# Optimization experiments

Measured on AMD Instinct MI355X. Metric: run time of the kernel, lower is better.

## Reference

```python
import jax, jax.numpy as jnp
import numpy as np

N_NODES = 50000
N_EDGES = 625000
D = 128


def setup_inputs() -> dict:
    key = jax.random.key(0)
    kx, ks, kr, kw, kb = jax.random.split(key, 5)
    x = jax.random.normal(kx, (N_NODES, D), dtype=jnp.float32)
    senders = jax.random.randint(ks, (N_EDGES,), 0, N_NODES, dtype=jnp.int64)
    receivers = jax.random.randint(kr, (N_EDGES,), 0, N_NODES, dtype=jnp.int64)
    # nn.Linear(2*D, D): weight [D, 2*D], bias [D]
    lim = 1.0 / np.sqrt(2 * D)
    W = jax.random.uniform(kw, (D, 2 * D), minval=-lim, maxval=lim, dtype=jnp.float32)
    b = jax.random.uniform(kb, (D,), minval=-lim, maxval=lim, dtype=jnp.float32)
    return {"x": x, "senders": senders, "receivers": receivers, "n_nodes": N_NODES, "W": W, "b": b}


def reference(x, senders, receivers, n_nodes, W, b):
    # Add self loops (with_self=True)
    self_idx = jnp.arange(n_nodes, dtype=senders.dtype)
    s = jnp.concatenate([senders, self_idx])   # [E + N]
    r = jnp.concatenate([receivers, self_idx]) # [E + N]

    ones = jnp.ones(r.shape[0], dtype=x.dtype)
    # degree_norm=True branch (note: mirrors the original's naming exactly:
    # 'out_degree' counted over receivers, 'in_degree' over senders)
    out_degree = jax.ops.segment_sum(ones, r, num_segments=n_nodes)  # [N]
    in_degree = jax.ops.segment_sum(ones, s, num_segments=n_nodes)   # [N]
    out_degree_norm = jax.lax.rsqrt(jnp.maximum(out_degree, 1.0))
    in_degree_norm = jax.lax.rsqrt(jnp.maximum(in_degree, 1.0))

    # Gather sender embeddings, scale, scatter-add to receivers
    sender_emb = x[s] * out_degree_norm[s][:, None]  # [E+N, D]
    aggregated = jax.ops.segment_sum(sender_emb, r, num_segments=n_nodes)  # [N, D]

    # edge_count over receivers == out_degree (same scatter), clamped
    edge_count = jnp.maximum(out_degree, 1.0)
    aggregated = aggregated / edge_count[:, None]
    aggregated = aggregated * in_degree_norm[:, None]

    combined = jnp.concatenate([x, aggregated], axis=1)  # [N, 2D]
    return combined @ W.T + b
```

## Files before the change

### kernel.cpp

```cpp
#include <hip/hip_runtime.h>

#define DIM 128
#define BM 128
#define BK 32
#define PAD 16

typedef __attribute__((ext_vector_type(8))) short short8;
typedef __attribute__((ext_vector_type(4))) float f32x4;

__device__ __forceinline__ unsigned short f2bf(float f) {
    unsigned int b = __float_as_uint(f);
    return (unsigned short)((b + 0x7fffu + ((b >> 16) & 1u)) >> 16);
}
__device__ __forceinline__ float bf_lo(unsigned int u) {
    return __uint_as_float(u << 16);
}
__device__ __forceinline__ float bf_hi(unsigned int u) {
    return __uint_as_float(u & 0xffff0000u);
}
__device__ __forceinline__ uint2 pack4(float4 v) {
    uint2 r;
    r.x = (unsigned int)f2bf(v.x) | ((unsigned int)f2bf(v.y) << 16);
    r.y = (unsigned int)f2bf(v.z) | ((unsigned int)f2bf(v.w) << 16);
    return r;
}

__global__ void prep_kernel(const float4* __restrict__ x4,
                            const float4* __restrict__ W4,
                            const int* __restrict__ senders,
                            const int* __restrict__ receivers,
                            uint2* __restrict__ xb4,
                            uint2* __restrict__ Wb4,
                            int* __restrict__ cnt_r_pad,
                            int* __restrict__ cnt_s_pad,
                            int* __restrict__ rank,
                            int nx4, int nw4, int E) {
    int i = blockIdx.x * blockDim.x + threadIdx.x;
    if (i < nw4) Wb4[i] = pack4(W4[i]);
    if (i < E) {
        int r = receivers[i];
        int s = senders[i];
        rank[i] = atomicAdd(&cnt_r_pad[r * PAD], 1);
        atomicAdd(&cnt_s_pad[s * PAD], 1);
    }
    if (i < nx4) xb4[i] = pack4(x4[i]);
}

__global__ __launch_bounds__(256) void scan_phase_a(const int* __restrict__ cnt_r_pad,
                                                    int* __restrict__ bsum, int N) {
    __shared__ int red[256];
    int t = threadIdx.x;
    int i = blockIdx.x * 256 + t;
    red[t] = (i < N) ? cnt_r_pad[i * PAD] : 0;
    __syncthreads();
    for (int s = 128; s > 0; s >>= 1) {
        if (t < s) red[t] += red[t + s];
        __syncthreads();
    }
    if (t == 0) bsum[blockIdx.x] = red[0];
}

__global__ __launch_bounds__(256) void scan_phase_b(const int* __restrict__ bsum,
                                                    int* __restrict__ boff, int NB) {
    __shared__ int sh[256];
    int t = threadIdx.x;
    int v = (t < NB) ? bsum[t] : 0;
    sh[t] = v;
    __syncthreads();
    for (int off = 1; off < 256; off <<= 1) {
        int u = (t >= off) ? sh[t - off] : 0;
        __syncthreads();
        sh[t] += u;
        __syncthreads();
    }
    if (t < NB) boff[t] = sh[t] - v;
}

__global__ __launch_bounds__(256) void scan_phase_c(const int* __restrict__ cnt_r_pad,
                                                    const int* __restrict__ cnt_s_pad,
                                                    const int* __restrict__ boff,
                                                    int* __restrict__ row_start,
                                                    float* __restrict__ sscale,
                                                    float2* __restrict__ fin2,
                                                    int N) {
    __shared__ int sh[256];
    int t = threadIdx.x;
    int i = blockIdx.x * 256 + t;
    int v = (i < N) ? cnt_r_pad[i * PAD] : 0;
    sh[t] = v;
    __syncthreads();
    for (int off = 1; off < 256; off <<= 1) {
        int u = (t >= off) ? sh[t - off] : 0;
        __syncthreads();
        sh[t] += u;
        __syncthreads();
    }
    if (i < N) {
        int excl = sh[t] - v + boff[blockIdx.x];
        row_start[i] = excl;
        if (i == N - 1) row_start[N] = excl + v;
        float od = (float)(v + 1);
        float onorm = rsqrtf(od);
        sscale[i] = onorm;
        int ds = cnt_s_pad[i * PAD];
        fin2[i] = make_float2(onorm, rsqrtf((float)(ds + 1)) / od);
    }
}

__global__ void fill_kernel(const int* __restrict__ senders,
                            const int* __restrict__ receivers,
                            const int* __restrict__ row_start,
                            const int* __restrict__ rank,
                            int* __restrict__ edge_src,
                            int E) {
    int e = blockIdx.x * blockDim.x + threadIdx.x;
    if (e < E) {
        int r = receivers[e];
        edge_src[row_start[r] + rank[e]] = senders[e];
    }
}

__global__ __launch_bounds__(256) void gather_kernel(
        const unsigned int* __restrict__ xb,
        const int* __restrict__ edge_src,
        const int* __restrict__ row_start,
        const float* __restrict__ sscale,
        const float2* __restrict__ fin2,
        unsigned int* __restrict__ aggb,
        int N) {
    int lane = threadIdx.x & 63;
    int n = (blockIdx.x * blockDim.x + threadIdx.x) >> 6;
    if (n >= N) return;

    int start = row_start[n];
    int deg   = row_start[n + 1] - start;
    float ax = 0.f, ay = 0.f;

    for (int base = 0; base < deg; base += 64) {
        int cnt = deg - base; if (cnt > 64) cnt = 64;
        int   src = 0;
        float sc  = 0.f;
        if (lane < cnt) {
            src = edge_src[start + base + lane];
            sc  = sscale[src];
        }
        int j = 0;
        for (; j + 8 <= cnt; j += 8) {
            int ss[8]; float cc[8]; unsigned int uu[8];
#pragma unroll
            for (int q = 0; q < 8; q++) {
                ss[q] = __shfl(src, j + q);
                cc[q] = __shfl(sc,  j + q);
            }
#pragma unroll
            for (int q = 0; q < 8; q++)
                uu[q] = xb[(size_t)ss[q] * 64 + lane];
#pragma unroll
            for (int q = 0; q < 8; q++) {
                ax += bf_lo(uu[q]) * cc[q];
                ay += bf_hi(uu[q]) * cc[q];
            }
        }
        for (; j < cnt; j++) {
            int   s = __shfl(src, j);
            float c = __shfl(sc, j);
            unsigned int u = xb[(size_t)s * 64 + lane];
            ax += bf_lo(u) * c;
            ay += bf_hi(u) * c;
        }
    }

    float2 f = fin2[n];
    unsigned int u = xb[(size_t)n * 64 + lane];
    ax = (ax + bf_lo(u) * f.x) * f.y;
    ay = (ay + bf_hi(u) * f.x) * f.y;
    aggb[(size_t)n * 64 + lane] =
        (unsigned int)f2bf(ax) | ((unsigned int)f2bf(ay) << 16);
}

__global__ __launch_bounds__(256) void gemm_kernel(
        const unsigned short* __restrict__ x_bf,
        const unsigned short* __restrict__ agg_bf,
        const unsigned short* __restrict__ W_bf,
        const float* __restrict__ bias,
        float* __restrict__ out, int N) {
    __shared__ unsigned short As[BM * BK];
    __shared__ unsigned short Bs[DIM * BK];

    int t    = threadIdx.x;
    int lane = t & 63;
    int w    = t >> 6;
    int wr   = w >> 1, wc = w & 1;
    int row0 = blockIdx.x * BM;

    f32x4 acc[4][4];
#pragma unroll
    for (int i = 0; i < 4; i++)
#pragma unroll
        for (int j = 0; j < 4; j++) acc[i][j] = (f32x4){0.f, 0.f, 0.f, 0.f};

    for (int kt = 0; kt < 8; kt++) {
        const unsigned short* src = (kt < 4) ? x_bf : agg_bf;
        int k0 = (kt & 3) * BK;
#pragma unroll
        for (int p = 0; p < 2; p++) {
            int idx = p * 256 + t;
            int row = idx >> 2;
            int ch  = idx & 3;
            uint4 v = *(const uint4*)&src[(size_t)(row0 + row) * 128 + k0 + ch * 8];
            *(uint4*)&As[row * BK + ch * 8] = v;
        }
#pragma unroll
        for (int p = 0; p < 2; p++) {
            int idx = p * 256 + t;
            int n   = idx >> 2;
            int ch  = idx & 3;
            uint4 v = *(const uint4*)&W_bf[(size_t)n * 256 + kt * BK + ch * 8];
            *(uint4*)&Bs[n * BK + ch * 8] = v;
        }
        __syncthreads();

        short8 a[4], b[4];
#pragma unroll
        for (int i = 0; i < 4; i++)
            a[i] = *(const short8*)&As[(wr * 64 + i * 16 + (lane & 15)) * BK + (lane >> 4) * 8];
#pragma unroll
        for (int j = 0; j < 4; j++)
            b[j] = *(const short8*)&Bs[(wc * 64 + j * 16 + (lane & 15)) * BK + (lane >> 4) * 8];
#pragma unroll
        for (int i = 0; i < 4; i++)
#pragma unroll
            for (int j = 0; j < 4; j++)
                acc[i][j] = __builtin_amdgcn_mfma_f32_16x16x32_bf16(a[i], b[j], acc[i][j], 0, 0, 0);
        __syncthreads();
    }

    int cq = lane >> 4;
    int cl = lane & 15;
#pragma unroll
    for (int j = 0; j < 4; j++) {
        int col = wc * 64 + j * 16 + cl;
        float bb = bias[col];
#pragma unroll
        for (int i = 0; i < 4; i++) {
            int rbase = row0 + wr * 64 + i * 16 + cq * 4;
#pragma unroll
            for (int r = 0; r < 4; r++) {
                int row = rbase + r;
                if (row < N) out[(size_t)row * DIM + col] = acc[i][j][r] + bb;
            }
        }
    }
}

extern "C" void kernel_launch(void* const* d_in, const int* in_sizes, int n_in,
                              void* d_out, int out_size, void* d_ws, size_t ws_size,
                              hipStream_t stream) {
    const float* x         = (const float*)d_in[0];
    const int*   senders   = (const int*)d_in[1];
    const int*   receivers = (const int*)d_in[2];
    const float* W         = (const float*)d_in[4];
    const float* bias      = (const float*)d_in[5];
    float*       out       = (float*)d_out;

    int N  = in_sizes[0] / DIM;
    int E  = in_sizes[1];
    int NB = (N + 255) / 256;
    int NP = ((N + BM - 1) / BM) * BM;

    char* ws = (char*)d_ws;
    size_t off = 0;
    #define WS_ALLOC(ptrtype, name, bytes) \
        ptrtype name = (ptrtype)(ws + off); off += (((size_t)(bytes)) + 255) & ~(size_t)255;
    WS_ALLOC(int*,            cnt_r_pad, (size_t)N * PAD * 4)
    WS_ALLOC(int*,            cnt_s_pad, (size_t)N * PAD * 4)
    WS_ALLOC(int*,            row_start, (size_t)(N + 1) * 4)
    WS_ALLOC(int*,            rank,      (size_t)E * 4)
    WS_ALLOC(int*,            bsum,      4096)
    WS_ALLOC(int*,            boff,      4096)
    WS_ALLOC(int*,            edge_src,  (size_t)E * 4)
    WS_ALLOC(float*,          sscale,    (size_t)N * 4)
    WS_ALLOC(float2*,         fin2,      (size_t)N * 8)
    WS_ALLOC(unsigned short*, x_bf,      (size_t)NP * DIM * 2)
    WS_ALLOC(unsigned short*, agg_bf,    (size_t)NP * DIM * 2)
    WS_ALLOC(unsigned short*, W_bf,      (size_t)DIM * 256 * 2)
    #undef WS_ALLOC

    hipMemsetAsync(ws, 0, (size_t)N * PAD * 8, stream);

    int nx4 = N * 32;
    int nw4 = DIM * 256 / 4;
    int prep_threads = (nx4 > E) ? nx4 : E;
    prep_kernel<<<(prep_threads + 255) / 256, 256, 0, stream>>>(
        (const float4*)x, (const float4*)W, senders, receivers,
        (uint2*)x_bf, (uint2*)W_bf, cnt_r_pad, cnt_s_pad, rank, nx4, nw4, E);
    scan_phase_a<<<NB, 256, 0, stream>>>(cnt_r_pad, bsum, N);
    scan_phase_b<<<1, 256, 0, stream>>>(bsum, boff, NB);
    scan_phase_c<<<NB, 256, 0, stream>>>(cnt_r_pad, cnt_s_pad, boff,
                                         row_start, sscale, fin2, N);
    fill_kernel<<<(E + 255) / 256, 256, 0, stream>>>(senders, receivers,
                                                     row_start, rank, edge_src, E);
    gather_kernel<<<(N * 64 + 255) / 256, 256, 0, stream>>>(
        (const unsigned int*)x_bf, edge_src, row_start, sscale, fin2,
        (unsigned int*)agg_bf, N);
    gemm_kernel<<<(N + BM - 1) / BM, 256, 0, stream>>>(
        x_bf, agg_bf, W_bf, bias, out, N);
}
```

Baseline: 199.5 us.

## Replace global atomic CSR build with two-level binned counting sort

Builds the receiver-sorted CSR with a coarse bin histogram and scatter using shared-memory atomics, then a per-bin fine sort, instead of global per-node atomics with padded counters plus a three-phase scan. Sender degrees are counted the same way. A prescale pass folds the sender normalisation into a bf16 copy of x, so the gather no longer loads a per-edge scale. The aim is to remove contended global atomics and the scattered scale loads. In exchange it adds more kernel launches and an extra rounding of the scaled features. It also packs sender ids into 16 bits, which assumes N is at most 65536.

```diff
diff --git a/kernel.cpp b/kernel.cpp
--- a/kernel.cpp
+++ b/kernel.cpp
@@ -3,7 +3,8 @@
 #define DIM 128
 #define BM 128
 #define BK 32
-#define PAD 16
+#define BINSZ 128
+#define EPB 2048
 
 typedef __attribute__((ext_vector_type(8))) short short8;
 typedef __attribute__((ext_vector_type(4))) float f32x4;
@@ -12,120 +13,188 @@
     unsigned int b = __float_as_uint(f);
     return (unsigned short)((b + 0x7fffu + ((b >> 16) & 1u)) >> 16);
 }
-__device__ __forceinline__ float bf_lo(unsigned int u) {
-    return __uint_as_float(u << 16);
-}
-__device__ __forceinline__ float bf_hi(unsigned int u) {
-    return __uint_as_float(u & 0xffff0000u);
+__device__ __forceinline__ float bf_lo(unsigned int u) { return __uint_as_float(u << 16); }
+__device__ __forceinline__ float bf_hi(unsigned int u) { return __uint_as_float(u & 0xffff0000u); }
+__device__ __forceinline__ unsigned int pack2(float a, float b) {
+    return (unsigned int)f2bf(a) | ((unsigned int)f2bf(b) << 16);
 }
 __device__ __forceinline__ uint2 pack4(float4 v) {
-    uint2 r;
-    r.x = (unsigned int)f2bf(v.x) | ((unsigned int)f2bf(v.y) << 16);
-    r.y = (unsigned int)f2bf(v.z) | ((unsigned int)f2bf(v.w) << 16);
-    return r;
-}
-
-__global__ void prep_kernel(const float4* __restrict__ x4,
-                            const float4* __restrict__ W4,
-                            const int* __restrict__ senders,
-                            const int* __restrict__ receivers,
-                            uint2* __restrict__ xb4,
-                            uint2* __restrict__ Wb4,
-                            int* __restrict__ cnt_r_pad,
-                            int* __restrict__ cnt_s_pad,
-                            int* __restrict__ rank,
-                            int nx4, int nw4, int E) {
+    uint2 r; r.x = pack2(v.x, v.y); r.y = pack2(v.z, v.w); return r;
+}
+
+__global__ void convert_kernel(const float4* __restrict__ x4,
+                               const float4* __restrict__ W4,
+                               uint2* __restrict__ xb4,
+                               uint2* __restrict__ Wb4,
+                               int nx4, int nw4) {
     int i = blockIdx.x * blockDim.x + threadIdx.x;
+    if (i < nx4) xb4[i] = pack4(x4[i]);
     if (i < nw4) Wb4[i] = pack4(W4[i]);
-    if (i < E) {
-        int r = receivers[i];
-        int s = senders[i];
-        rank[i] = atomicAdd(&cnt_r_pad[r * PAD], 1);
-        atomicAdd(&cnt_s_pad[s * PAD], 1);
-    }
-    if (i < nx4) xb4[i] = pack4(x4[i]);
-}
-
-__global__ __launch_bounds__(256) void scan_phase_a(const int* __restrict__ cnt_r_pad,
-                                                    int* __restrict__ bsum, int N) {
-    __shared__ int red[256];
+}
+
+__global__ __launch_bounds__(256) void coarse_hist_kernel(
+        const int* __restrict__ senders, const int* __restrict__ receivers,
+        int* __restrict__ ccr, int* __restrict__ ccs, int E, int nbin) {
+    __shared__ int hr[512], hs[512];
     int t = threadIdx.x;
-    int i = blockIdx.x * 256 + t;
-    red[t] = (i < N) ? cnt_r_pad[i * PAD] : 0;
-    __syncthreads();
-    for (int s = 128; s > 0; s >>= 1) {
-        if (t < s) red[t] += red[t + s];
-        __syncthreads();
-    }
-    if (t == 0) bsum[blockIdx.x] = red[0];
-}
-
-__global__ __launch_bounds__(256) void scan_phase_b(const int* __restrict__ bsum,
-                                                    int* __restrict__ boff, int NB) {
-    __shared__ int sh[256];
+    for (int b = t; b < nbin; b += 256) { hr[b] = 0; hs[b] = 0; }
+    __syncthreads();
+    int base = blockIdx.x * EPB;
+    for (int k = 0; k < EPB; k += 256) {
+        int e = base + k + t;
+        if (e < E) {
+            atomicAdd(&hr[receivers[e] >> 7], 1);
+            atomicAdd(&hs[senders[e] >> 7], 1);
+        }
+    }
+    __syncthreads();
+    for (int b = t; b < nbin; b += 256) {
+        if (hr[b]) atomicAdd(&ccr[b], hr[b]);
+        if (hs[b]) atomicAdd(&ccs[b], hs[b]);
+    }
+}
+
+__global__ __launch_bounds__(512) void coarse_scan_kernel(
+        const int* __restrict__ ccr, const int* __restrict__ ccs,
+        int* __restrict__ startR, int* __restrict__ startS,
+        int* __restrict__ curR, int* __restrict__ curS,
+        int* __restrict__ row_start, int nbin, int N, int E) {
+    __shared__ int sh[1024];
     int t = threadIdx.x;
-    int v = (t < NB) ? bsum[t] : 0;
-    sh[t] = v;
-    __syncthreads();
-    for (int off = 1; off < 256; off <<= 1) {
-        int u = (t >= off) ? sh[t - off] : 0;
-        __syncthreads();
-        sh[t] += u;
-        __syncthreads();
-    }
-    if (t < NB) boff[t] = sh[t] - v;
-}
-
-__global__ __launch_bounds__(256) void scan_phase_c(const int* __restrict__ cnt_r_pad,
-                                                    const int* __restrict__ cnt_s_pad,
-                                                    const int* __restrict__ boff,
-                                                    int* __restrict__ row_start,
-                                                    float* __restrict__ sscale,
-                                                    float2* __restrict__ fin2,
-                                                    int N) {
-    __shared__ int sh[256];
+    int vr = (t < nbin) ? ccr[t] : 0;
+    int vs = (t < nbin) ? ccs[t] : 0;
+    sh[t] = vr; sh[512 + t] = vs;
+    __syncthreads();
+    for (int off = 1; off < 512; off <<= 1) {
+        int ur = (t >= off) ? sh[t - off] : 0;
+        int us = (t >= off) ? sh[512 + t - off] : 0;
+        __syncthreads();
+        sh[t] += ur; sh[512 + t] += us;
+        __syncthreads();
+    }
+    if (t < nbin) {
+        int er = sh[t] - vr, es = sh[512 + t] - vs;
+        startR[t] = er; curR[t] = er;
+        startS[t] = es; curS[t] = es;
+    }
+    if (t == 0) { startR[nbin] = E; startS[nbin] = E; row_start[N] = E; }
+}
+
+__global__ __launch_bounds__(256) void coarse_scatter_kernel(
+        const int* __restrict__ senders, const int* __restrict__ receivers,
+        int* __restrict__ curR, int* __restrict__ curS,
+        unsigned int* __restrict__ bucket_r,
+        int* __restrict__ bucket_s,
+        int E, int nbin) {
+    __shared__ int hr[512], hs[512];
+    __shared__ int br_[512], bs_[512];
     int t = threadIdx.x;
-    int i = blockIdx.x * 256 + t;
-    int v = (i < N) ? cnt_r_pad[i * PAD] : 0;
-    sh[t] = v;
-    __syncthreads();
-    for (int off = 1; off < 256; off <<= 1) {
-        int u = (t >= off) ? sh[t - off] : 0;
-        __syncthreads();
-        sh[t] += u;
-        __syncthreads();
-    }
-    if (i < N) {
-        int excl = sh[t] - v + boff[blockIdx.x];
-        row_start[i] = excl;
-        if (i == N - 1) row_start[N] = excl + v;
-        float od = (float)(v + 1);
-        float onorm = rsqrtf(od);
-        sscale[i] = onorm;
-        int ds = cnt_s_pad[i * PAD];
-        fin2[i] = make_float2(onorm, rsqrtf((float)(ds + 1)) / od);
-    }
-}
-
-__global__ void fill_kernel(const int* __restrict__ senders,
-                            const int* __restrict__ receivers,
-                            const int* __restrict__ row_start,
-                            const int* __restrict__ rank,
-                            int* __restrict__ edge_src,
-                            int E) {
-    int e = blockIdx.x * blockDim.x + threadIdx.x;
-    if (e < E) {
-        int r = receivers[e];
-        edge_src[row_start[r] + rank[e]] = senders[e];
-    }
+    for (int b = t; b < nbin; b += 256) { hr[b] = 0; hs[b] = 0; }
+    __syncthreads();
+    int base = blockIdx.x * EPB;
+    for (int k = 0; k < EPB; k += 256) {
+        int e = base + k + t;
+        if (e < E) {
+            atomicAdd(&hr[receivers[e] >> 7], 1);
+            atomicAdd(&hs[senders[e] >> 7], 1);
+        }
+    }
+    __syncthreads();
+    for (int b = t; b < nbin; b += 256) {
+        br_[b] = hr[b] ? atomicAdd(&curR[b], hr[b]) : 0;
+        bs_[b] = hs[b] ? atomicAdd(&curS[b], hs[b]) : 0;
+    }
+    __syncthreads();
+    for (int k = 0; k < EPB; k += 256) {
+        int e = base + k + t;
+        if (e < E) {
+            int s = senders[e], r = receivers[e];
+            int pr = atomicAdd(&br_[r >> 7], 1);
+            bucket_r[pr] = ((unsigned int)(r & 127) << 16) | (unsigned int)s;
+            int ps = atomicAdd(&bs_[s >> 7], 1);
+            bucket_s[ps] = s;
+        }
+    }
+}
+
+__global__ __launch_bounds__(256) void fine_r_kernel(
+        const unsigned int* __restrict__ bucket_r,
+        const int* __restrict__ startR,
+        int* __restrict__ edge_src,
+        int* __restrict__ row_start, int N) {
+    __shared__ int fine[BINSZ];
+    __shared__ int fstart[BINSZ];
+    int b = blockIdx.x, t = threadIdx.x;
+    if (t < BINSZ) fine[t] = 0;
+    __syncthreads();
+    int lo = startR[b], hi = startR[b + 1];
+    for (int i = lo + t; i < hi; i += 256)
+        atomicAdd(&fine[bucket_r[i] >> 16], 1);
+    __syncthreads();
+    if (t < BINSZ) fstart[t] = fine[t];
+    __syncthreads();
+    for (int off = 1; off < BINSZ; off <<= 1) {
+        int u = (t < BINSZ && t >= off) ? fstart[t - off] : 0;
+        __syncthreads();
+        if (t < BINSZ) fstart[t] += u;
+        __syncthreads();
+    }
+    if (t < BINSZ) {
+        int excl = fstart[t] - fine[t];
+        int node = b * BINSZ + t;
+        if (node < N) row_start[node] = lo + excl;
+        fstart[t] = excl;
+    }
+    __syncthreads();
+    for (int i = lo + t; i < hi; i += 256) {
+        unsigned int u = bucket_r[i];
+        int pos = atomicAdd(&fstart[u >> 16], 1);
+        edge_src[lo + pos] = (int)(u & 0xFFFFu);
+    }
+}
+
+__global__ __launch_bounds__(256) void fine_s_kernel(
+        const int* __restrict__ bucket_s,
+        const int* __restrict__ startS,
+        int* __restrict__ cnt_s, int N) {
+    __shared__ int fine[BINSZ];
+    int b = blockIdx.x, t = threadIdx.x;
+    if (t < BINSZ) fine[t] = 0;
+    __syncthreads();
+    int lo = startS[b], hi = startS[b + 1];
+    for (int i = lo + t; i < hi; i += 256)
+        atomicAdd(&fine[bucket_s[i] & 127], 1);
+    __syncthreads();
+    if (t < BINSZ) {
+        int node = b * BINSZ + t;
+        if (node < N) cnt_s[node] = fine[t];
+    }
+}
+
+__global__ __launch_bounds__(256) void prescale_kernel(
+        const uint2* __restrict__ xb2,
+        const int* __restrict__ row_start,
+        const int* __restrict__ cnt_s,
+        uint2* __restrict__ xs2,
+        float* __restrict__ fs, int N) {
+    int i = blockIdx.x * blockDim.x + threadIdx.x;
+    int n = i >> 5, c = i & 31;
+    if (n >= N) return;
+    float od = (float)(row_start[n + 1] - row_start[n] + 1);
+    float sc = rsqrtf(od);
+    uint2 u = xb2[(size_t)n * 32 + c];
+    uint2 o;
+    o.x = pack2(bf_lo(u.x) * sc, bf_hi(u.x) * sc);
+    o.y = pack2(bf_lo(u.y) * sc, bf_hi(u.y) * sc);
+    xs2[(size_t)n * 32 + c] = o;
+    if (c == 0) fs[n] = rsqrtf((float)(cnt_s[n] + 1)) / od;
 }
 
 __global__ __launch_bounds__(256) void gather_kernel(
-        const unsigned int* __restrict__ xb,
+        const unsigned int* __restrict__ xs,
         const int* __restrict__ edge_src,
         const int* __restrict__ row_start,
-        const float* __restrict__ sscale,
-        const float2* __restrict__ fin2,
+        const float* __restrict__ fs,
         unsigned int* __restrict__ aggb,
         int N) {
     int lane = threadIdx.x & 63;
@@ -138,44 +207,30 @@
 
     for (int base = 0; base < deg; base += 64) {
         int cnt = deg - base; if (cnt > 64) cnt = 64;
-        int   src = 0;
-        float sc  = 0.f;
-        if (lane < cnt) {
-            src = edge_src[start + base + lane];
-            sc  = sscale[src];
-        }
+        int src = 0;
+        if (lane < cnt) src = edge_src[start + base + lane];
         int j = 0;
         for (; j + 8 <= cnt; j += 8) {
-            int ss[8]; float cc[8]; unsigned int uu[8];
-#pragma unroll
-            for (int q = 0; q < 8; q++) {
-                ss[q] = __shfl(src, j + q);
-                cc[q] = __shfl(sc,  j + q);
-            }
-#pragma unroll
-            for (int q = 0; q < 8; q++)
-                uu[q] = xb[(size_t)ss[q] * 64 + lane];
-#pragma unroll
-            for (int q = 0; q < 8; q++) {
-                ax += bf_lo(uu[q]) * cc[q];
-                ay += bf_hi(uu[q]) * cc[q];
-            }
+            int ss[8]; unsigned int uu[8];
+#pragma unroll
+            for (int q = 0; q < 8; q++) ss[q] = __shfl(src, j + q);
+#pragma unroll
+            for (int q = 0; q < 8; q++) uu[q] = xs[(size_t)ss[q] * 64 + lane];
+#pragma unroll
+            for (int q = 0; q < 8; q++) { ax += bf_lo(uu[q]); ay += bf_hi(uu[q]); }
         }
         for (; j < cnt; j++) {
-            int   s = __shfl(src, j);
-            float c = __shfl(sc, j);
-            unsigned int u = xb[(size_t)s * 64 + lane];
-            ax += bf_lo(u) * c;
-            ay += bf_hi(u) * c;
-        }
-    }
-
-    float2 f = fin2[n];
-    unsigned int u = xb[(size_t)n * 64 + lane];
-    ax = (ax + bf_lo(u) * f.x) * f.y;
-    ay = (ay + bf_hi(u) * f.x) * f.y;
-    aggb[(size_t)n * 64 + lane] =
-        (unsigned int)f2bf(ax) | ((unsigned int)f2bf(ay) << 16);
+            int s = __shfl(src, j);
+            unsigned int u = xs[(size_t)s * 64 + lane];
+            ax += bf_lo(u); ay += bf_hi(u);
+        }
+    }
+
+    float f = fs[n];
+    unsigned int u = xs[(size_t)n * 64 + lane];
+    ax = (ax + bf_lo(u)) * f;
+    ay = (ay + bf_hi(u)) * f;
+    aggb[(size_t)n * 64 + lane] = pack2(ax, ay);
 }
 
 __global__ __launch_bounds__(256) void gemm_kernel(
@@ -263,45 +318,53 @@
     const float* bias      = (const float*)d_in[5];
     float*       out       = (float*)d_out;
 
-    int N  = in_sizes[0] / DIM;
-    int E  = in_sizes[1];
-    int NB = (N + 255) / 256;
-    int NP = ((N + BM - 1) / BM) * BM;
+    int N    = in_sizes[0] / DIM;
+    int E    = in_sizes[1];
+    int nbin = (N + BINSZ - 1) / BINSZ;
+    int NAB  = (E + EPB - 1) / EPB;
+    int NP   = ((N + BM - 1) / BM) * BM;
 
     char* ws = (char*)d_ws;
     size_t off = 0;
     #define WS_ALLOC(ptrtype, name, bytes) \
         ptrtype name = (ptrtype)(ws + off); off += (((size_t)(bytes)) + 255) & ~(size_t)255;
-    WS_ALLOC(int*,            cnt_r_pad, (size_t)N * PAD * 4)
-    WS_ALLOC(int*,            cnt_s_pad, (size_t)N * PAD * 4)
+    WS_ALLOC(int*,            ccr,       (size_t)nbin * 4)
+    WS_ALLOC(int*,            ccs,       (size_t)nbin * 4)
+    size_t zero_end = off;
+    WS_ALLOC(int*,            startR,    (size_t)(nbin + 1) * 4)
+    WS_ALLOC(int*,            startS,    (size_t)(nbin + 1) * 4)
+    WS_ALLOC(int*,            curR,      (size_t)nbin * 4)
+    WS_ALLOC(int*,            curS,      (size_t)nbin * 4)
     WS_ALLOC(int*,            row_start, (size_t)(N + 1) * 4)
-    WS_ALLOC(int*,            rank,      (size_t)E * 4)
-    WS_ALLOC(int*,            bsum,      4096)
-    WS_ALLOC(int*,            boff,      4096)
+    WS_ALLOC(int*,            cnt_s,     (size_t)N * 4)
+    WS_ALLOC(float*,          fs,        (size_t)N * 4)
     WS_ALLOC(int*,            edge_src,  (size_t)E * 4)
-    WS_ALLOC(float*,          sscale,    (size_t)N * 4)
-    WS_ALLOC(float2*,         fin2,      (size_t)N * 8)
     WS_ALLOC(unsigned short*, x_bf,      (size_t)NP * DIM * 2)
+    WS_ALLOC(unsigned short*, xs_bf,     (size_t)NP * DIM * 2)
     WS_ALLOC(unsigned short*, agg_bf,    (size_t)NP * DIM * 2)
     WS_ALLOC(unsigned short*, W_bf,      (size_t)DIM * 256 * 2)
     #undef WS_ALLOC
 
-    hipMemsetAsync(ws, 0, (size_t)N * PAD * 8, stream);
+    unsigned int* bucket_r = (unsigned int*)agg_bf;
+    int*          bucket_s = (int*)((char*)agg_bf + (((size_t)E * 4 + 255) & ~(size_t)255));
+
+    hipMemsetAsync(ws, 0, zero_end, stream);
 
     int nx4 = N * 32;
     int nw4 = DIM * 256 / 4;
-    int prep_threads = (nx4 > E) ? nx4 : E;
-    prep_kernel<<<(prep_threads + 255) / 256, 256, 0, stream>>>(
-        (const float4*)x, (const float4*)W, senders, receivers,
-        (uint2*)x_bf, (uint2*)W_bf, cnt_r_pad, cnt_s_pad, rank, nx4, nw4, E);
-    scan_phase_a<<<NB, 256, 0, stream>>>(cnt_r_pad, bsum, N);
-    scan_phase_b<<<1, 256, 0, stream>>>(bsum, boff, NB);
-    scan_phase_c<<<NB, 256, 0, stream>>>(cnt_r_pad, cnt_s_pad, boff,
-                                         row_start, sscale, fin2, N);
-    fill_kernel<<<(E + 255) / 256, 256, 0, stream>>>(senders, receivers,
-                                                     row_start, rank, edge_src, E);
+    convert_kernel<<<(nx4 + 255) / 256, 256, 0, stream>>>(
+        (const float4*)x, (const float4*)W, (uint2*)x_bf, (uint2*)W_bf, nx4, nw4);
+    coarse_hist_kernel<<<NAB, 256, 0, stream>>>(senders, receivers, ccr, ccs, E, nbin);
+    coarse_scan_kernel<<<1, 512, 0, stream>>>(ccr, ccs, startR, startS,
+                                              curR, curS, row_start, nbin, N, E);
+    coarse_scatter_kernel<<<NAB, 256, 0, stream>>>(senders, receivers, curR, curS,
+                                                   bucket_r, bucket_s, E, nbin);
+    fine_r_kernel<<<nbin, 256, 0, stream>>>(bucket_r, startR, edge_src, row_start, N);
+    fine_s_kernel<<<nbin, 256, 0, stream>>>(bucket_s, startS, cnt_s, N);
+    prescale_kernel<<<(N * 32 + 255) / 256, 256, 0, stream>>>(
+        (const uint2*)x_bf, row_start, cnt_s, (uint2*)xs_bf, fs, N);
     gather_kernel<<<(N * 64 + 255) / 256, 256, 0, stream>>>(
-        (const unsigned int*)x_bf, edge_src, row_start, sscale, fin2,
+        (const unsigned int*)xs_bf, edge_src, row_start, fs,
         (unsigned int*)agg_bf, N);
     gemm_kernel<<<(N + BM - 1) / BM, 256, 0, stream>>>(
         x_bf, agg_bf, W_bf, bias, out, N);
```

After: 181.7 us. 8.9% less time.
